# Kernel optimization log

Measured on AMD Instinct MI355X. Metric: run time of the kernel, lower is better.

Reference implementation:

```python
import jax, jax.numpy as jnp
import numpy as np

B, S, D = 2, 512, 128      # batch, seq_len, d_att
DG, NG = 64, 2             # d_group, n_group = D // DG


def setup_inputs() -> dict:
    key = jax.random.key(0)
    ks = jax.random.split(key, 12)
    def w(k, shape, scale):
        return jax.random.normal(k, shape, dtype=jnp.float32) * scale
    proj_scale = 1.0 / D                      # xavier_uniform-ish std / sqrt(d_att)
    mlp1 = (2.0 / (DG + DG)) ** 0.5
    mlp2 = (2.0 / (DG + 16)) ** 0.5
    mlp3 = (2.0 / (16 + 1)) ** 0.5
    return {
        "x": w(ks[0], (B, S, D), 1.0),
        "positional_adding_bias": w(ks[1], (1, NG, 1, S, S), 1.0),
        "positional_multiplying_bias": jax.random.uniform(ks[2], (1, NG, 1, S, S), dtype=jnp.float32),
        "Wq": w(ks[3], (D, D), proj_scale),
        "Wk": w(ks[4], (D, D), proj_scale),
        "Wv": w(ks[5], (D, D), proj_scale),
        "W1": w(ks[6], (DG, DG), mlp1), "b1": jnp.zeros((DG,), jnp.float32),
        "W2": w(ks[7], (DG, 16), mlp2), "b2": jnp.zeros((16,), jnp.float32),
        "W3": w(ks[8], (16, 1), mlp3),  "b3": jnp.zeros((1,), jnp.float32),
    }


def reference(x, positional_adding_bias, positional_multiplying_bias,
              Wq, Wk, Wv, W1, b1, W2, b2, W3, b3):
    Q = x @ Wq   # [B,S,D]
    K = x @ Wk
    V = x @ Wv
    # pairwise Q-K differences, grouped: [B,S,S,NG,DG] (d_att split as n_group,d_group)
    diff = (Q[:, :, None, :] - K[:, None, :, :]).reshape(B, S, S, NG, DG)
    # per-group scoring MLP (Linear->ReLU x3, final width 1)
    h = jax.nn.relu(diff @ W1 + b1)
    h = jax.nn.relu(h @ W2 + b2)
    a = jax.nn.relu(h @ W3 + b3)                 # [B,S,S,NG,1]
    a = jnp.transpose(a, (0, 3, 4, 1, 2))        # [B,NG,1,S,S]
    a = a * positional_multiplying_bias + positional_adding_bias
    a = jax.nn.softmax(a, axis=-1)[:, :, 0]      # [B,NG,S,S], softmax over keys
    # NOTE: original reshapes V as (d_group, n_group) — faithful reproduction
    Vr = V.reshape(B, S, DG, NG)                 # [B,S,DG,NG]
    out = jnp.einsum('bisk,bkji->bsji', a, Vr)   # [B,S,DG,NG]
    return out.reshape(B, S, D)
```

## Files before the change

### kernel.cpp

```cpp
#include <hip/hip_runtime.h>

#define BQ 2
#define SQ 512
#define DQ 128
#define DGQ 64
#define NGQ 2

typedef float float2v __attribute__((ext_vector_type(2)));


__global__ __launch_bounds__(256) void proj_kernel(
    const float* __restrict__ x,
    const float* __restrict__ Wq, const float* __restrict__ Wk,
    const float* __restrict__ Wv,
    const float* __restrict__ W1, const float* __restrict__ b1,
    float* __restrict__ QW1, float* __restrict__ KW1, float* __restrict__ Vp)
{
    const int t = threadIdx.x;
    const int row = blockIdx.x;
    __shared__ float xs[DQ];
    __shared__ float part[3][2][DQ];
    __shared__ float qs[DQ], ks[DQ];

    if (t < DQ) xs[t] = x[(size_t)row * DQ + t];
    __syncthreads();

    const int f = t & 127, h = t >> 7;
    float aq = 0.f, ak = 0.f, av = 0.f;
    const int d0 = h * 64;
    #pragma unroll 8
    for (int d = 0; d < 64; ++d) {
        const float xv = xs[d0 + d];
        const size_t o = (size_t)(d0 + d) * DQ + f;
        aq = fmaf(xv, Wq[o], aq);
        ak = fmaf(xv, Wk[o], ak);
        av = fmaf(xv, Wv[o], av);
    }
    part[0][h][f] = aq; part[1][h][f] = ak; part[2][h][f] = av;
    __syncthreads();

    if (t < DQ) {
        qs[t] = part[0][0][t] + part[0][1][t];
        const float v = part[2][0][t] + part[2][1][t];
        Vp[((size_t)row * NGQ + (t & 1)) * DGQ + (t >> 1)] = v;
    } else {
        const int f2 = t - DQ;
        ks[f2] = part[1][0][f2] + part[1][1][f2];
    }
    __syncthreads();

    const int fb = t & 127, side = t >> 7;
    const int g = fb >> 6, c = fb & 63;
    const float* src = side ? ks : qs;
    float acc = side ? 0.f : b1[c];
    #pragma unroll 8
    for (int e = 0; e < 64; ++e)
        acc = fmaf(src[g * 64 + e], W1[e * DGQ + c], acc);
    (side ? KW1 : QW1)[(size_t)row * DQ + fb] = acc;
}

__global__ __launch_bounds__(512) void attn_kernel(
    const float* __restrict__ QW1, const float* __restrict__ KW1,
    const float* __restrict__ Vp,
    const float* __restrict__ W2, const float* __restrict__ b2,
    const float* __restrict__ W3, const float* __restrict__ b3,
    const float* __restrict__ pos_add, const float* __restrict__ pos_mul,
    float* __restrict__ out)
{
    const int t = threadIdx.x;
    const int ipair = blockIdx.x & 255;
    const int g = (blockIdx.x >> 8) & 1;
    const int b = blockIdx.x >> 9;
    const int i0 = ipair * 2;

    __shared__ __align__(16) float qsl[2][DGQ];
    __shared__ __align__(8)  float sc[SQ * 2];
    __shared__ float redm[2][8], reds[2][8];
    __shared__ float avs[2][8][DGQ];

    if (t < 2 * DGQ) {
        const int qq = t >> 6, e = t & 63;
        qsl[qq][e] = QW1[((size_t)(b * SQ + i0 + qq)) * DQ + g * DGQ + e];
    }
    const size_t bo0 = ((size_t)g * SQ + i0) * SQ + t;
    const float pm0 = pos_mul[bo0],      pa0 = pos_add[bo0];
    const float pm1 = pos_mul[bo0 + SQ], pa1 = pos_add[bo0 + SQ];
    __syncthreads();

    const float4* krow = reinterpret_cast<const float4*>(
        KW1 + ((size_t)(b * SQ + t)) * DQ + g * DGQ);
    const float2v* qv0 = reinterpret_cast<const float2v*>(&qsl[0][0]);
    const float2v* qv1 = reinterpret_cast<const float2v*>(&qsl[1][0]);
    const float2v* b2v = reinterpret_cast<const float2v*>(b2);

    float2v acc0[8], acc1[8];
    #pragma unroll
    for (int o = 0; o < 8; ++o) { acc0[o] = b2v[o]; acc1[o] = b2v[o]; }

    #pragma unroll 2
    for (int c4 = 0; c4 < 16; ++c4) {
        const float4 kv = krow[c4];
        const float2v k01 = {kv.x, kv.y}, k23 = {kv.z, kv.w};
        const float2v d01a = qv0[c4 * 2] - k01,     d23a = qv0[c4 * 2 + 1] - k23;
        const float2v d01b = qv1[c4 * 2] - k01,     d23b = qv1[c4 * 2 + 1] - k23;
        const float ha0 = fmaxf(d01a.x, 0.f), ha1 = fmaxf(d01a.y, 0.f);
        const float ha2 = fmaxf(d23a.x, 0.f), ha3 = fmaxf(d23a.y, 0.f);
        const float hb0 = fmaxf(d01b.x, 0.f), hb1 = fmaxf(d01b.y, 0.f);
        const float hb2 = fmaxf(d23b.x, 0.f), hb3 = fmaxf(d23b.y, 0.f);
        const float2v* w2r = reinterpret_cast<const float2v*>(W2 + c4 * 64);
        #pragma unroll
        for (int o = 0; o < 8; ++o) {
            const float2v w0 = w2r[o], w1 = w2r[8 + o];
            const float2v w2_ = w2r[16 + o], w3_ = w2r[24 + o];
            acc0[o] += ha0 * w0;  acc0[o] += ha1 * w1;
            acc0[o] += ha2 * w2_; acc0[o] += ha3 * w3_;
            acc1[o] += hb0 * w0;  acc1[o] += hb1 * w1;
            acc1[o] += hb2 * w2_; acc1[o] += hb3 * w3_;
        }
    }
    float a0 = b3[0], a1 = b3[0];
    #pragma unroll
    for (int o = 0; o < 8; ++o) {
        a0 = fmaf(fmaxf(acc0[o].x, 0.f), W3[2 * o], a0);
        a0 = fmaf(fmaxf(acc0[o].y, 0.f), W3[2 * o + 1], a0);
        a1 = fmaf(fmaxf(acc1[o].x, 0.f), W3[2 * o], a1);
        a1 = fmaf(fmaxf(acc1[o].y, 0.f), W3[2 * o + 1], a1);
    }
    const float logit0 = fmaf(fmaxf(a0, 0.f), pm0, pa0);
    const float logit1 = fmaf(fmaxf(a1, 0.f), pm1, pa1);

    float m0 = logit0, m1 = logit1;
    #pragma unroll
    for (int off = 32; off > 0; off >>= 1) {
        m0 = fmaxf(m0, __shfl_xor(m0, off));
        m1 = fmaxf(m1, __shfl_xor(m1, off));
    }
    const int wave = t >> 6;
    if ((t & 63) == 0) { redm[0][wave] = m0; redm[1][wave] = m1; }
    __syncthreads();
    float M0 = redm[0][0], M1 = redm[1][0];
    #pragma unroll
    for (int w = 1; w < 8; ++w) {
        M0 = fmaxf(M0, redm[0][w]); M1 = fmaxf(M1, redm[1][w]);
    }
    const float e0 = __expf(logit0 - M0);
    const float e1 = __expf(logit1 - M1);
    *reinterpret_cast<float2v*>(&sc[t * 2]) = float2v{e0, e1};
    float s0 = e0, s1 = e1;
    #pragma unroll
    for (int off = 32; off > 0; off >>= 1) {
        s0 += __shfl_xor(s0, off);
        s1 += __shfl_xor(s1, off);
    }
    if ((t & 63) == 0) { reds[0][wave] = s0; reds[1][wave] = s1; }
    __syncthreads();
    float S0 = 0.f, S1 = 0.f;
    #pragma unroll
    for (int w = 0; w < 8; ++w) { S0 += reds[0][w]; S1 += reds[1][w]; }
    const float inv0 = 1.f / S0, inv1 = 1.f / S1;

    const int dim = t & 63, q = t >> 6;
    const float* vbase = Vp + (((size_t)(b * SQ + q * 64)) * NGQ + g) * DGQ + dim;
    float2v accv = {0.f, 0.f};
    #pragma unroll 8
    for (int k = 0; k < 64; ++k) {
        const float v = vbase[(size_t)k * (NGQ * DGQ)];
        const float2v sv = *reinterpret_cast<const float2v*>(&sc[(q * 64 + k) * 2]);
        accv += v * sv;
    }
    avs[0][q][dim] = accv.x;
    avs[1][q][dim] = accv.y;
    __syncthreads();
    if (t < 2 * DGQ) {
        const int qq = t >> 6, d = t & 63;
        float sum = 0.f;
        #pragma unroll
        for (int w = 0; w < 8; ++w) sum += avs[qq][w][d];
        out[((size_t)(b * SQ + i0 + qq)) * DQ + d * NGQ + g] =
            sum * (qq ? inv1 : inv0);
    }
}

extern "C" void kernel_launch(void* const* d_in, const int* in_sizes, int n_in,
                              void* d_out, int out_size, void* d_ws, size_t ws_size,
                              hipStream_t stream) {
    const float* x       = (const float*)d_in[0];
    const float* pos_add = (const float*)d_in[1];
    const float* pos_mul = (const float*)d_in[2];
    const float* Wq      = (const float*)d_in[3];
    const float* Wk      = (const float*)d_in[4];
    const float* Wv      = (const float*)d_in[5];
    const float* W1      = (const float*)d_in[6];
    const float* b1      = (const float*)d_in[7];
    const float* W2      = (const float*)d_in[8];
    const float* b2      = (const float*)d_in[9];
    const float* W3      = (const float*)d_in[10];
    const float* b3      = (const float*)d_in[11];
    float* out = (float*)d_out;

    float* ws  = (float*)d_ws;
    float* QW1 = ws;
    float* KW1 = ws + 131072;
    float* Vp  = ws + 262144;

    proj_kernel<<<BQ * SQ, 256, 0, stream>>>(x, Wq, Wk, Wv, W1, b1,
                                             QW1, KW1, Vp);
    attn_kernel<<<BQ * NGQ * SQ / 2, 512, 0, stream>>>(QW1, KW1, Vp, W2, b2,
                                                       W3, b3, pos_add, pos_mul,
                                                       out);
}
```

Measured before the change: 129.6 us.

## Compute pairwise scoring MLP layer with fp16 MFMA instead of scalar FMAs

The W2 layer of the per-pair scoring MLP now runs on MFMA 16x16x32 f16 instructions, with relu(q-k) fragments converted to half precision and W2 held as B fragments. The W3 projection is done with a 16-lane shuffle reduction. Each block now handles one query row instead of two, which doubles the grid. This aims to move the dominant S*S*64*16 FLOP work onto matrix cores, at the cost of fp16 rounding of the activations and weights and of reloading K rows per query.

Result: no change. 132.2 us (+2.0%).

```diff
diff --git a/kernel.cpp b/kernel.cpp
--- a/kernel.cpp
+++ b/kernel.cpp
@@ -7,6 +7,8 @@
 #define NGQ 2
 
 typedef float float2v __attribute__((ext_vector_type(2)));
+typedef float float4v __attribute__((ext_vector_type(4)));
+typedef _Float16 half8 __attribute__((ext_vector_type(8)));
 
 
 __global__ __launch_bounds__(256) void proj_kernel(
@@ -68,116 +70,117 @@
     float* __restrict__ out)
 {
     const int t = threadIdx.x;
-    const int ipair = blockIdx.x & 255;
-    const int g = (blockIdx.x >> 8) & 1;
-    const int b = blockIdx.x >> 9;
-    const int i0 = ipair * 2;
-
-    __shared__ __align__(16) float qsl[2][DGQ];
-    __shared__ __align__(8)  float sc[SQ * 2];
-    __shared__ float redm[2][8], reds[2][8];
-    __shared__ float avs[2][8][DGQ];
-
-    if (t < 2 * DGQ) {
-        const int qq = t >> 6, e = t & 63;
-        qsl[qq][e] = QW1[((size_t)(b * SQ + i0 + qq)) * DQ + g * DGQ + e];
-    }
-    const size_t bo0 = ((size_t)g * SQ + i0) * SQ + t;
-    const float pm0 = pos_mul[bo0],      pa0 = pos_add[bo0];
-    const float pm1 = pos_mul[bo0 + SQ], pa1 = pos_add[bo0 + SQ];
-    __syncthreads();
-
-    const float4* krow = reinterpret_cast<const float4*>(
-        KW1 + ((size_t)(b * SQ + t)) * DQ + g * DGQ);
-    const float2v* qv0 = reinterpret_cast<const float2v*>(&qsl[0][0]);
-    const float2v* qv1 = reinterpret_cast<const float2v*>(&qsl[1][0]);
-    const float2v* b2v = reinterpret_cast<const float2v*>(b2);
-
-    float2v acc0[8], acc1[8];
-    #pragma unroll
-    for (int o = 0; o < 8; ++o) { acc0[o] = b2v[o]; acc1[o] = b2v[o]; }
-
-    #pragma unroll 2
-    for (int c4 = 0; c4 < 16; ++c4) {
-        const float4 kv = krow[c4];
-        const float2v k01 = {kv.x, kv.y}, k23 = {kv.z, kv.w};
-        const float2v d01a = qv0[c4 * 2] - k01,     d23a = qv0[c4 * 2 + 1] - k23;
-        const float2v d01b = qv1[c4 * 2] - k01,     d23b = qv1[c4 * 2 + 1] - k23;
-        const float ha0 = fmaxf(d01a.x, 0.f), ha1 = fmaxf(d01a.y, 0.f);
-        const float ha2 = fmaxf(d23a.x, 0.f), ha3 = fmaxf(d23a.y, 0.f);
-        const float hb0 = fmaxf(d01b.x, 0.f), hb1 = fmaxf(d01b.y, 0.f);
-        const float hb2 = fmaxf(d23b.x, 0.f), hb3 = fmaxf(d23b.y, 0.f);
-        const float2v* w2r = reinterpret_cast<const float2v*>(W2 + c4 * 64);
-        #pragma unroll
-        for (int o = 0; o < 8; ++o) {
-            const float2v w0 = w2r[o], w1 = w2r[8 + o];
-            const float2v w2_ = w2r[16 + o], w3_ = w2r[24 + o];
-            acc0[o] += ha0 * w0;  acc0[o] += ha1 * w1;
-            acc0[o] += ha2 * w2_; acc0[o] += ha3 * w3_;
-            acc1[o] += hb0 * w0;  acc1[o] += hb1 * w1;
-            acc1[o] += hb2 * w2_; acc1[o] += hb3 * w3_;
+    const int lane = t & 63, wv = t >> 6;
+    const int n = lane & 15, q = lane >> 4;
+    const int i = blockIdx.x & (SQ - 1);
+    const int g = (blockIdx.x >> 9) & 1;
+    const int b = blockIdx.x >> 10;
+
+    __shared__ __align__(16) float sc[SQ];
+    __shared__ float redm[8], reds[8];
+    __shared__ float avs[8][DGQ];
+
+    const size_t bo = ((size_t)g * SQ + i) * SQ + t;
+    const float pmv = pos_mul[bo], pav = pos_add[bo];
+
+    half8 bfrag[2];
+    #pragma unroll
+    for (int kb = 0; kb < 2; ++kb)
+        #pragma unroll
+        for (int j = 0; j < 8; ++j)
+            bfrag[kb][j] = (_Float16)W2[(kb * 32 + q * 8 + j) * 16 + n];
+
+    const float* qrow = QW1 + ((size_t)(b * SQ + i)) * DQ + g * DGQ;
+    float4 qf[4];
+    #pragma unroll
+    for (int kb = 0; kb < 2; ++kb) {
+        qf[kb * 2 + 0] = *(const float4*)(qrow + kb * 32 + q * 8);
+        qf[kb * 2 + 1] = *(const float4*)(qrow + kb * 32 + q * 8 + 4);
+    }
+    const float accInit = b2[n];
+    const float w3n = W3[n];
+    const float b3v = b3[0];
+
+    const float* kbase = KW1 + ((size_t)(b * SQ)) * DQ + g * DGQ;
+
+    #pragma unroll
+    for (int tt = 0; tt < 4; ++tt) {
+        const int m0 = wv * 64 + tt * 16;
+        const float* krow = kbase + (size_t)(m0 + n) * DQ;
+        half8 afrag[2];
+        #pragma unroll
+        for (int kb = 0; kb < 2; ++kb) {
+            const float4 k0 = *(const float4*)(krow + kb * 32 + q * 8);
+            const float4 k1 = *(const float4*)(krow + kb * 32 + q * 8 + 4);
+            const float4 q0 = qf[kb * 2], q1 = qf[kb * 2 + 1];
+            afrag[kb][0] = (_Float16)fmaxf(q0.x - k0.x, 0.f);
+            afrag[kb][1] = (_Float16)fmaxf(q0.y - k0.y, 0.f);
+            afrag[kb][2] = (_Float16)fmaxf(q0.z - k0.z, 0.f);
+            afrag[kb][3] = (_Float16)fmaxf(q0.w - k0.w, 0.f);
+            afrag[kb][4] = (_Float16)fmaxf(q1.x - k1.x, 0.f);
+            afrag[kb][5] = (_Float16)fmaxf(q1.y - k1.y, 0.f);
+            afrag[kb][6] = (_Float16)fmaxf(q1.z - k1.z, 0.f);
+            afrag[kb][7] = (_Float16)fmaxf(q1.w - k1.w, 0.f);
         }
-    }
-    float a0 = b3[0], a1 = b3[0];
-    #pragma unroll
-    for (int o = 0; o < 8; ++o) {
-        a0 = fmaf(fmaxf(acc0[o].x, 0.f), W3[2 * o], a0);
-        a0 = fmaf(fmaxf(acc0[o].y, 0.f), W3[2 * o + 1], a0);
-        a1 = fmaf(fmaxf(acc1[o].x, 0.f), W3[2 * o], a1);
-        a1 = fmaf(fmaxf(acc1[o].y, 0.f), W3[2 * o + 1], a1);
-    }
-    const float logit0 = fmaf(fmaxf(a0, 0.f), pm0, pa0);
-    const float logit1 = fmaf(fmaxf(a1, 0.f), pm1, pa1);
-
-    float m0 = logit0, m1 = logit1;
-    #pragma unroll
-    for (int off = 32; off > 0; off >>= 1) {
-        m0 = fmaxf(m0, __shfl_xor(m0, off));
-        m1 = fmaxf(m1, __shfl_xor(m1, off));
-    }
-    const int wave = t >> 6;
-    if ((t & 63) == 0) { redm[0][wave] = m0; redm[1][wave] = m1; }
-    __syncthreads();
-    float M0 = redm[0][0], M1 = redm[1][0];
-    #pragma unroll
-    for (int w = 1; w < 8; ++w) {
-        M0 = fmaxf(M0, redm[0][w]); M1 = fmaxf(M1, redm[1][w]);
-    }
-    const float e0 = __expf(logit0 - M0);
-    const float e1 = __expf(logit1 - M1);
-    *reinterpret_cast<float2v*>(&sc[t * 2]) = float2v{e0, e1};
-    float s0 = e0, s1 = e1;
-    #pragma unroll
-    for (int off = 32; off > 0; off >>= 1) {
-        s0 += __shfl_xor(s0, off);
-        s1 += __shfl_xor(s1, off);
-    }
-    if ((t & 63) == 0) { reds[0][wave] = s0; reds[1][wave] = s1; }
-    __syncthreads();
-    float S0 = 0.f, S1 = 0.f;
-    #pragma unroll
-    for (int w = 0; w < 8; ++w) { S0 += reds[0][w]; S1 += reds[1][w]; }
-    const float inv0 = 1.f / S0, inv1 = 1.f / S1;
-
-    const int dim = t & 63, q = t >> 6;
-    const float* vbase = Vp + (((size_t)(b * SQ + q * 64)) * NGQ + g) * DGQ + dim;
-    float2v accv = {0.f, 0.f};
-    #pragma unroll 8
-    for (int k = 0; k < 64; ++k) {
-        const float v = vbase[(size_t)k * (NGQ * DGQ)];
-        const float2v sv = *reinterpret_cast<const float2v*>(&sc[(q * 64 + k) * 2]);
-        accv += v * sv;
-    }
-    avs[0][q][dim] = accv.x;
-    avs[1][q][dim] = accv.y;
-    __syncthreads();
-    if (t < 2 * DGQ) {
-        const int qq = t >> 6, d = t & 63;
+        float4v acc = {accInit, accInit, accInit, accInit};
+        acc = __builtin_amdgcn_mfma_f32_16x16x32_f16(afrag[0], bfrag[0], acc, 0, 0, 0);
+        acc = __builtin_amdgcn_mfma_f32_16x16x32_f16(afrag[1], bfrag[1], acc, 0, 0, 0);
+
+        float tr0 = fmaxf(acc[0], 0.f) * w3n;
+        float tr1 = fmaxf(acc[1], 0.f) * w3n;
+        float tr2 = fmaxf(acc[2], 0.f) * w3n;
+        float tr3 = fmaxf(acc[3], 0.f) * w3n;
+        #pragma unroll
+        for (int off = 1; off < 16; off <<= 1) {
+            tr0 += __shfl_xor(tr0, off);
+            tr1 += __shfl_xor(tr1, off);
+            tr2 += __shfl_xor(tr2, off);
+            tr3 += __shfl_xor(tr3, off);
+        }
+        if (n == 0) {
+            float4 av4;
+            av4.x = fmaxf(tr0 + b3v, 0.f);
+            av4.y = fmaxf(tr1 + b3v, 0.f);
+            av4.z = fmaxf(tr2 + b3v, 0.f);
+            av4.w = fmaxf(tr3 + b3v, 0.f);
+            *(float4*)&sc[m0 + q * 4] = av4;
+        }
+    }
+    __syncthreads();
+
+    const float logit = fmaf(sc[t], pmv, pav);
+    float m = logit;
+    #pragma unroll
+    for (int off = 32; off > 0; off >>= 1) m = fmaxf(m, __shfl_xor(m, off));
+    if (lane == 0) redm[wv] = m;
+    __syncthreads();
+    float M = redm[0];
+    #pragma unroll
+    for (int w = 1; w < 8; ++w) M = fmaxf(M, redm[w]);
+    const float e = __expf(logit - M);
+    float s = e;
+    #pragma unroll
+    for (int off = 32; off > 0; off >>= 1) s += __shfl_xor(s, off);
+    if (lane == 0) reds[wv] = s;
+    sc[t] = e;
+    __syncthreads();
+    float S = 0.f;
+    #pragma unroll
+    for (int w = 0; w < 8; ++w) S += reds[w];
+    const float inv = 1.f / S;
+
+    const float* vbase = Vp + (((size_t)(b * SQ + wv * 64)) * NGQ + g) * DGQ + lane;
+    float accv = 0.f;
+    #pragma unroll 16
+    for (int k = 0; k < 64; ++k)
+        accv = fmaf(sc[wv * 64 + k], vbase[(size_t)k * (NGQ * DGQ)], accv);
+    avs[wv][lane] = accv;
+    __syncthreads();
+    if (t < DGQ) {
         float sum = 0.f;
         #pragma unroll
-        for (int w = 0; w < 8; ++w) sum += avs[qq][w][d];
-        out[((size_t)(b * SQ + i0 + qq)) * DQ + d * NGQ + g] =
-            sum * (qq ? inv1 : inv0);
+        for (int w = 0; w < 8; ++w) sum += avs[w][t];
+        out[((size_t)(b * SQ + i)) * DQ + t * NGQ + g] = sum * inv;
     }
 }
 
@@ -205,7 +208,7 @@
 
     proj_kernel<<<BQ * SQ, 256, 0, stream>>>(x, Wq, Wk, Wv, W1, b1,
                                              QW1, KW1, Vp);
-    attn_kernel<<<BQ * NGQ * SQ / 2, 512, 0, stream>>>(QW1, KW1, Vp, W2, b2,
-                                                       W3, b3, pos_add, pos_mul,
-                                                       out);
+    attn_kernel<<<BQ * NGQ * SQ, 512, 0, stream>>>(QW1, KW1, Vp, W2, b2,
+                                                   W3, b3, pos_add, pos_mul,
+                                                   out);
 }
```
